# Kernel optimization log

Hardware: AMD Instinct MI355X
Metric: run time of the kernel (lower is better)

## Reference

```python
import jax, jax.numpy as jnp
import numpy as np

EPS = 1e-5
TOP_K = 2

def _conv(x, w, pad):
    # x: [B,Cin,H,W], w: [Cout,Cin,kh,kw]
    return jax.lax.conv_general_dilated(
        x, w, (1, 1), [(pad, pad), (pad, pad)],
        dimension_numbers=('NCHW', 'OIHW', 'NCHW'))

def _bn_eval(x, scale, bias):
    # BatchNorm2d in eval mode with running_mean=0, running_var=1
    inv = scale / jnp.sqrt(1.0 + EPS)
    return x * inv[None, :, None, None] + bias[None, :, None, None]

def setup_inputs() -> dict:
    key = jax.random.key(0)
    ks = jax.random.split(key, 8)
    B, C, O, H, W, E, HID = 16, 256, 256, 56, 56, 8, 512  # HID = int(2.0 * C)
    g = lambda k, shape, f: jax.random.normal(k, shape, jnp.float32) * f
    return {
        'x': jax.random.normal(ks[0], (B, C, H, W), jnp.float32),
        # EfficientSpatialRouter: global-avg-pool -> 1x1 conv to E logits
        'router_w': g(ks[1], (E, C), 0.01),
        'router_b': jnp.zeros((E,), jnp.float32),
        # shared expert: 1x1 conv -> BN -> SiLU
        'shared_w': g(ks[2], (O, C, 1, 1), 0.05),
        'shared_scale': jnp.ones((O,), jnp.float32),
        'shared_bias': jnp.zeros((O,), jnp.float32),
        # SimpleExpert per expert: conv3x3 C->HID, BN, SiLU, conv1x1 HID->O, BN
        'w1': g(ks[3], (E, HID, C, 3, 3), 0.02),
        'bn1_scale': jnp.ones((E, HID), jnp.float32),
        'bn1_bias': jnp.zeros((E, HID), jnp.float32),
        'w2': g(ks[4], (E, O, HID, 1, 1), 0.02),
        'bn2_scale': jnp.ones((E, O), jnp.float32),
        'bn2_bias': jnp.zeros((E, O), jnp.float32),
    }

def reference(x, router_w, router_b, shared_w, shared_scale, shared_bias,
              w1, bn1_scale, bn1_bias, w2, bn2_scale, bn2_bias):
    E = router_w.shape[0]
    # --- routing: pooled features -> logits -> softmax -> top-k renormalized ---
    pooled = x.mean(axis=(2, 3))                          # [B,C]
    logits = pooled @ router_w.T + router_b               # [B,E]
    probs = jax.nn.softmax(logits, axis=-1)
    topk_vals, topk_idx = jax.lax.top_k(probs, TOP_K)     # [B,K]
    weights = topk_vals / topk_vals.sum(axis=-1, keepdims=True)
    # --- shared expert ---
    shared = jax.nn.silu(_bn_eval(_conv(x, shared_w, 0), shared_scale, shared_bias))
    # --- expert dispatch/combine (dense-masked equivalent of gather + index_add) ---
    expert_out = jnp.zeros_like(shared)
    for e in range(E):  # fixed small expert count
        gate = jnp.sum(weights * (topk_idx == e), axis=-1)  # [B], 0 if not routed
        h = jax.nn.silu(_bn_eval(_conv(x, w1[e], 1), bn1_scale[e], bn1_bias[e]))
        y = _bn_eval(_conv(h, w2[e], 0), bn2_scale[e], bn2_bias[e])
        expert_out = expert_out + gate[:, None, None, None] * y
    # residual since in_channels == out_channels
    return shared + expert_out + x
```

## Files before the change

kernel.cpp:

```cpp
#include <hip/hip_runtime.h>
#include <hip/hip_bf16.h>

#define B_ 16
#define C_ 256
#define O_ 256
#define P_ 3136
#define E_ 8
#define HID_ 512
#define EPS_ 1e-5f

typedef __attribute__((ext_vector_type(8))) short bf16x8;
typedef __attribute__((ext_vector_type(4))) float f32x4;
typedef __hip_bfloat16 bf16;

__device__ __forceinline__ void gl2lds16(const bf16* g, bf16* l) {
  __builtin_amdgcn_global_load_lds((const __attribute__((address_space(1))) void*)g,
                                   (__attribute__((address_space(3))) void*)l,
                                   16, 0, 0);
}

__global__ __launch_bounds__(256) void xT_kernel(const float* __restrict__ x,
                                                 bf16* __restrict__ xT,
                                                 float* __restrict__ pooled) {
  __shared__ float tile[64][65];
  const int p0 = blockIdx.x * 64, c0 = blockIdx.y * 64, b = blockIdx.z;
  const int t = threadIdx.x;
#pragma unroll
  for (int j = 0; j < 16; ++j) {
    int idx = t + j * 256;
    int cl = idx >> 6, pl = idx & 63;
    tile[cl][pl] = x[(size_t)(b * C_ + c0 + cl) * P_ + p0 + pl];
  }
  __syncthreads();
#pragma unroll
  for (int j = 0; j < 16; ++j) {
    int idx = t + j * 256;
    int pl = idx >> 6, cl = idx & 63;
    xT[(size_t)(b * P_ + p0 + pl) * C_ + c0 + cl] = __float2bfloat16(tile[cl][pl]);
  }
  if (t < 64) {
    float s = 0.f;
#pragma unroll 8
    for (int pl = 0; pl < 64; ++pl) s += tile[t][pl];
    atomicAdd(&pooled[b * C_ + c0 + t], s * (1.0f / P_));
  }
}

__global__ __launch_bounds__(256) void w1cvt_kernel(const float* __restrict__ w1,
                                                    const float* __restrict__ bn1_scale,
                                                    bf16* __restrict__ w1b) {
  const int eh = blockIdx.x;
  const int e = eh >> 9, hid = eh & 511;
  __shared__ float buf[2304];
  const float* src = w1 + (size_t)eh * 2304;
  const int t = threadIdx.x;
  for (int i = t; i < 2304; i += 256) buf[i] = src[i];
  __syncthreads();
  const float inv = bn1_scale[eh] * (1.0f / sqrtf(1.0f + EPS_));
  for (int i = t; i < 2304; i += 256) {
    int rs = i >> 8, c = i & 255;
    w1b[((size_t)(e * 9 + rs) * HID_ + hid) * C_ + c] = __float2bfloat16(buf[c * 9 + rs] * inv);
  }
}

__global__ __launch_bounds__(256) void w2cvt_kernel(const float* __restrict__ w2,
                                                    const float* __restrict__ bn2_scale,
                                                    bf16* __restrict__ w2b) {
  const int i = blockIdx.x * 256 + threadIdx.x;
  const int eo = i >> 9;
  w2b[i] = __float2bfloat16(w2[i] * (bn2_scale[eo] * (1.0f / sqrtf(1.0f + EPS_))));
}

__global__ __launch_bounds__(256) void wshcvt_kernel(const float* __restrict__ wsh,
                                                     const float* __restrict__ sscale,
                                                     bf16* __restrict__ wshb) {
  const int i = blockIdx.x * 256 + threadIdx.x;
  wshb[i] = __float2bfloat16(wsh[i] * (sscale[i >> 8] * (1.0f / sqrtf(1.0f + EPS_))));
}

__global__ __launch_bounds__(256) void router_kernel(const float* __restrict__ pooled,
                                                     const float* __restrict__ rw,
                                                     const float* __restrict__ rb,
                                                     const float* __restrict__ bn2_bias,
                                                     int* __restrict__ ridx,
                                                     float* __restrict__ rwt,
                                                     float* __restrict__ bsum) {
  __shared__ float lp[B_ * C_];
  __shared__ float llog[B_ * E_];
  __shared__ int lidx[B_ * 2];
  __shared__ float lw[B_ * 2];
  const int t = threadIdx.x;
  for (int i = t; i < B_ * C_; i += 256) lp[i] = pooled[i];
  __syncthreads();
  if (t < B_ * E_) {
    int b = t >> 3, e = t & 7;
    float s = rb[e];
    for (int c = 0; c < C_; ++c) s += lp[b * C_ + c] * rw[e * C_ + c];
    llog[t] = s;
  }
  __syncthreads();
  if (t < B_) {
    float pr[E_];
    float m = -1e30f;
    for (int e = 0; e < E_; ++e) { pr[e] = llog[t * E_ + e]; m = fmaxf(m, pr[e]); }
    float s = 0.f;
    for (int e = 0; e < E_; ++e) { pr[e] = __expf(pr[e] - m); s += pr[e]; }
    const float is = 1.f / s;
    for (int e = 0; e < E_; ++e) pr[e] *= is;
    int i0 = 0; float v0 = pr[0];
    for (int e = 1; e < E_; ++e) if (pr[e] > v0) { v0 = pr[e]; i0 = e; }
    int i1 = -1; float v1 = -1.f;
    for (int e = 0; e < E_; ++e) if (e != i0 && pr[e] > v1) { v1 = pr[e]; i1 = e; }
    const float wsum = 1.f / (v0 + v1);
    ridx[t * 2] = i0; ridx[t * 2 + 1] = i1;
    rwt[t * 2] = v0 * wsum; rwt[t * 2 + 1] = v1 * wsum;
    lidx[t * 2] = i0; lidx[t * 2 + 1] = i1;
    lw[t * 2] = v0 * wsum; lw[t * 2 + 1] = v1 * wsum;
  }
  __syncthreads();
  for (int i = t; i < B_ * O_; i += 256) {
    int b = i >> 8, o = i & 255;
    bsum[i] = lw[b * 2] * bn2_bias[lidx[b * 2] * O_ + o]
            + lw[b * 2 + 1] * bn2_bias[lidx[b * 2 + 1] * O_ + o];
  }
}

__global__ __launch_bounds__(256) void conv1_kernel(
    const bf16* __restrict__ xT, const bf16* __restrict__ w1b,
    const float* __restrict__ bn1_bias, const int* __restrict__ ridx,
    const float* __restrict__ rwt, const bf16* __restrict__ zp,
    bf16* __restrict__ h) {
  __shared__ __align__(16) bf16 ldsA[2][128 * 32];
  __shared__ __align__(16) bf16 ldsB[2][128 * 32];
  const int t = threadIdx.x;
  const int p0 = blockIdx.x * 128;
  const int h0 = blockIdx.y * 128;
  const int bs = blockIdx.z;
  const int b = bs >> 1;
  const int e = ridx[bs];
  const float wk = rwt[bs];

  const int lane = t & 63, wv = t >> 6;
  const int wm = wv >> 1, wn = wv & 1;
  const int r16 = lane & 15, q = lane >> 4;
  const int kslot = (q ^ (r16 & 3)) * 8;

  const int rA = t >> 2;
  const int cSw = ((t & 3) ^ (rA & 3)) * 8;
  const int pA0 = p0 + rA, pA1 = pA0 + 64;
  const int yA0 = pA0 / 56, xA0 = pA0 - yA0 * 56;
  const int yA1 = pA1 / 56, xA1 = pA1 - yA1 * 56;
  const bool vP1 = (pA1 < P_);
  const bf16* xb = xT + (size_t)b * P_ * C_ + cSw;
  const bf16* wb = w1b + ((size_t)(e * 9) * HID_ + h0 + rA) * C_ + cSw;

  f32x4 acc[4][4] = {};

#define STAGE(buf, s) { \
    const int tap_ = (s) >> 3, c0k_ = ((s) & 7) * 32; \
    const int dr_ = tap_ / 3 - 1, dc_ = tap_ % 3 - 1; \
    const int off_ = dr_ * 56 + dc_; \
    const bool v0_ = ((unsigned)(yA0 + dr_) < 56u) & ((unsigned)(xA0 + dc_) < 56u); \
    const bool v1_ = vP1 & ((unsigned)(yA1 + dr_) < 56u) & ((unsigned)(xA1 + dc_) < 56u); \
    const bf16* a0_ = v0_ ? xb + (size_t)(pA0 + off_) * C_ + c0k_ : zp; \
    const bf16* a1_ = v1_ ? xb + (size_t)(pA1 + off_) * C_ + c0k_ : zp; \
    const bf16* b_ = wb + (size_t)(tap_ * HID_) * C_ + c0k_; \
    gl2lds16(a0_, ldsA[buf] + t * 8); \
    gl2lds16(a1_, ldsA[buf] + 2048 + t * 8); \
    gl2lds16(b_, ldsB[buf] + t * 8); \
    gl2lds16(b_ + 64 * C_, ldsB[buf] + 2048 + t * 8); \
  }

  STAGE(0, 0);
  __syncthreads();
  for (int s = 0; s < 72; ++s) {
    const int cur = s & 1;
    if (s < 71) STAGE(cur ^ 1, s + 1);
    const bf16* lA = ldsA[cur];
    const bf16* lB = ldsB[cur];
    bf16x8 af[4], bfr[4];
#pragma unroll
    for (int i = 0; i < 4; ++i) {
      af[i]  = *(const bf16x8*)(lA + (wm * 64 + i * 16 + r16) * 32 + kslot);
      bfr[i] = *(const bf16x8*)(lB + (wn * 64 + i * 16 + r16) * 32 + kslot);
    }
    __builtin_amdgcn_s_setprio(1);
#pragma unroll
    for (int mi = 0; mi < 4; ++mi)
#pragma unroll
      for (int ni = 0; ni < 4; ++ni)
        acc[mi][ni] = __builtin_amdgcn_mfma_f32_16x16x32_bf16(af[mi], bfr[ni], acc[mi][ni], 0, 0, 0);
    __builtin_amdgcn_s_setprio(0);
    if (s < 71) __syncthreads();
  }
#undef STAGE

  const int rowq = q * 4;
  float bias[4];
#pragma unroll
  for (int ni = 0; ni < 4; ++ni)
    bias[ni] = bn1_bias[e * HID_ + h0 + wn * 64 + ni * 16 + r16];
#pragma unroll
  for (int mi = 0; mi < 4; ++mi) {
#pragma unroll
    for (int i = 0; i < 4; ++i) {
      const int p = p0 + wm * 64 + mi * 16 + rowq + i;
      if (p < P_) {
        const size_t base = ((size_t)bs * P_ + p) * HID_;
#pragma unroll
        for (int ni = 0; ni < 4; ++ni) {
          const int hid = h0 + wn * 64 + ni * 16 + r16;
          float v = acc[mi][ni][i] + bias[ni];
          v = v / (1.f + __expf(-v));
          h[base + hid] = __float2bfloat16(wk * v);
        }
      }
    }
  }
}

__global__ __launch_bounds__(256) void combine_kernel(
    const bf16* __restrict__ xT, const bf16* __restrict__ h,
    const bf16* __restrict__ wshb, const bf16* __restrict__ w2b,
    const float* __restrict__ sbias, const float* __restrict__ bsum,
    const int* __restrict__ ridx, const float* __restrict__ x,
    const bf16* __restrict__ zp, float* __restrict__ out) {
  __shared__ __align__(16) bf16 ldsA[2][128 * 32];
  __shared__ __align__(16) bf16 ldsB[2][128 * 32];
  const int t = threadIdx.x;
  const int p0 = blockIdx.x * 128;
  const int o0 = blockIdx.y * 128;
  const int b = blockIdx.z;
  const int e0 = ridx[b * 2], e1 = ridx[b * 2 + 1];

  const int lane = t & 63, wv = t >> 6;
  const int wm = wv >> 1, wn = wv & 1;
  const int r16 = lane & 15, q = lane >> 4;
  const int kslot = (q ^ (r16 & 3)) * 8;

  const int rA = t >> 2;
  const int cSw = ((t & 3) ^ (rA & 3)) * 8;
  const int pB0 = p0 + rA, pB1 = pB0 + 64;
  const bool vB1 = (pB1 < P_);
  const bf16* shA = wshb + (size_t)(o0 + rA) * C_ + cSw;
  const bf16* xB = xT + (size_t)b * P_ * C_ + cSw;

  f32x4 acc[4][4] = {};

#define CSTAGE(buf, s) { \
    if ((s) < 8) { \
      const int c0k_ = (s) * 32; \
      gl2lds16(shA + c0k_, ldsA[buf] + t * 8); \
      gl2lds16(shA + 64 * C_ + c0k_, ldsA[buf] + 2048 + t * 8); \
      gl2lds16(xB + (size_t)pB0 * C_ + c0k_, ldsB[buf] + t * 8); \
      gl2lds16(vB1 ? xB + (size_t)pB1 * C_ + c0k_ : zp, ldsB[buf] + 2048 + t * 8); \
    } else { \
      const int ss_ = (s) - 8; const int slot_ = ss_ >> 4; const int c0k_ = (ss_ & 15) * 32; \
      const int ee_ = slot_ ? e1 : e0; \
      const bf16* wA_ = w2b + ((size_t)(ee_ * O_) + o0 + rA) * HID_ + c0k_ + cSw; \
      const bf16* hB_ = h + ((size_t)(b * 2 + slot_) * P_) * HID_ + c0k_ + cSw; \
      gl2lds16(wA_, ldsA[buf] + t * 8); \
      gl2lds16(wA_ + 64 * HID_, ldsA[buf] + 2048 + t * 8); \
      gl2lds16(hB_ + (size_t)pB0 * HID_, ldsB[buf] + t * 8); \
      gl2lds16(vB1 ? hB_ + (size_t)pB1 * HID_ : zp, ldsB[buf] + 2048 + t * 8); \
    } \
  }

  CSTAGE(0, 0);
  __syncthreads();
  for (int s = 0; s < 40; ++s) {
    const int cur = s & 1;
    if (s < 39) CSTAGE(cur ^ 1, s + 1);
    const bf16* lA = ldsA[cur];
    const bf16* lB = ldsB[cur];
    bf16x8 af[4], bfr[4];
#pragma unroll
    for (int i = 0; i < 4; ++i) {
      af[i]  = *(const bf16x8*)(lA + (wm * 64 + i * 16 + r16) * 32 + kslot);
      bfr[i] = *(const bf16x8*)(lB + (wn * 64 + i * 16 + r16) * 32 + kslot);
    }
    __builtin_amdgcn_s_setprio(1);
#pragma unroll
    for (int mi = 0; mi < 4; ++mi)
#pragma unroll
      for (int ni = 0; ni < 4; ++ni)
        acc[mi][ni] = __builtin_amdgcn_mfma_f32_16x16x32_bf16(af[mi], bfr[ni], acc[mi][ni], 0, 0, 0);
    __builtin_amdgcn_s_setprio(0);
    if (s == 7) {
      const int rowq_ = q * 4;
#pragma unroll
      for (int mi = 0; mi < 4; ++mi)
#pragma unroll
        for (int i = 0; i < 4; ++i) {
          const float bias_ = sbias[o0 + wm * 64 + mi * 16 + rowq_ + i];
#pragma unroll
          for (int ni = 0; ni < 4; ++ni) {
            float v = acc[mi][ni][i] + bias_;
            acc[mi][ni][i] = v / (1.f + __expf(-v));
          }
        }
    }
    if (s < 39) __syncthreads();
  }
#undef CSTAGE

  const int rowq = q * 4;
#pragma unroll
  for (int mi = 0; mi < 4; ++mi) {
#pragma unroll
    for (int i = 0; i < 4; ++i) {
      const int o = o0 + wm * 64 + mi * 16 + rowq + i;
      const float bb = bsum[b * O_ + o];
      const size_t orow = (size_t)(b * O_ + o) * P_;
#pragma unroll
      for (int ni = 0; ni < 4; ++ni) {
        const int p = p0 + wn * 64 + ni * 16 + r16;
        if (p < P_) out[orow + p] = acc[mi][ni][i] + bb + x[orow + p];
      }
    }
  }
}

constexpr size_t SZ_XT = (size_t)B_ * P_ * C_ * 2;
constexpr size_t SZ_W1B = (size_t)E_ * 9 * HID_ * C_ * 2;
constexpr size_t SZ_W2B = (size_t)E_ * O_ * HID_ * 2;
constexpr size_t SZ_WSHB = (size_t)O_ * C_ * 2;
constexpr size_t SZ_POOL = (size_t)B_ * C_ * 4;
constexpr size_t SZ_BSUM = (size_t)B_ * O_ * 4;
constexpr size_t SZ_H = (size_t)B_ * 2 * P_ * HID_ * 2;

constexpr size_t OFF_XT = 0;
constexpr size_t OFF_W1B = OFF_XT + SZ_XT;
constexpr size_t OFF_W2B = OFF_W1B + SZ_W1B;
constexpr size_t OFF_WSHB = OFF_W2B + SZ_W2B;
constexpr size_t OFF_POOL = OFF_WSHB + SZ_WSHB;
constexpr size_t OFF_RIDX = OFF_POOL + SZ_POOL;
constexpr size_t OFF_RWT = OFF_RIDX + 128;
constexpr size_t OFF_BSUM = OFF_RWT + 128;
constexpr size_t OFF_ZERO = OFF_BSUM + SZ_BSUM;
constexpr size_t OFF_H = OFF_ZERO + 1024;

extern "C" void kernel_launch(void* const* d_in, const int* in_sizes, int n_in,
                              void* d_out, int out_size, void* d_ws, size_t ws_size,
                              hipStream_t stream) {
  const float* x = (const float*)d_in[0];
  const float* router_w = (const float*)d_in[1];
  const float* router_b = (const float*)d_in[2];
  const float* shared_w = (const float*)d_in[3];
  const float* shared_scale = (const float*)d_in[4];
  const float* shared_bias = (const float*)d_in[5];
  const float* w1 = (const float*)d_in[6];
  const float* bn1_scale = (const float*)d_in[7];
  const float* bn1_bias = (const float*)d_in[8];
  const float* w2 = (const float*)d_in[9];
  const float* bn2_scale = (const float*)d_in[10];
  const float* bn2_bias = (const float*)d_in[11];
  float* out = (float*)d_out;
  char* ws = (char*)d_ws;

  bf16* xT = (bf16*)(ws + OFF_XT);
  bf16* w1b = (bf16*)(ws + OFF_W1B);
  bf16* w2b = (bf16*)(ws + OFF_W2B);
  bf16* wshb = (bf16*)(ws + OFF_WSHB);
  float* pooled = (float*)(ws + OFF_POOL);
  int* ridx = (int*)(ws + OFF_RIDX);
  float* rwt = (float*)(ws + OFF_RWT);
  float* bsum = (float*)(ws + OFF_BSUM);
  bf16* zp = (bf16*)(ws + OFF_ZERO);
  bf16* h = (bf16*)(ws + OFF_H);

  hipMemsetAsync(ws + OFF_POOL, 0, SZ_POOL, stream);
  hipMemsetAsync(ws + OFF_ZERO, 0, 1024, stream);

  xT_kernel<<<dim3(49, 4, 16), 256, 0, stream>>>(x, xT, pooled);
  w1cvt_kernel<<<E_ * HID_, 256, 0, stream>>>(w1, bn1_scale, w1b);
  w2cvt_kernel<<<(E_ * O_ * HID_) / 256, 256, 0, stream>>>(w2, bn2_scale, w2b);
  wshcvt_kernel<<<(O_ * C_) / 256, 256, 0, stream>>>(shared_w, shared_scale, wshb);
  router_kernel<<<1, 256, 0, stream>>>(pooled, router_w, router_b, bn2_bias, ridx, rwt, bsum);
  conv1_kernel<<<dim3(25, 4, 32), 256, 0, stream>>>(xT, w1b, bn1_bias, ridx, rwt, zp, h);
  combine_kernel<<<dim3(25, 2, 16), 256, 0, stream>>>(xT, h, wshb, w2b, shared_bias, bsum, ridx, x, zp, out);
}
```

Measured before the change: 675.5 us.

## Enlarge GEMM tiles, use K=64 triple-buffered LDS pipeline and XCD-aware block mapping

Both conv1 and combine kernels move to 512-thread blocks with larger output tiles: 256x128 in conv1, and all 256 output channels x 128 pixels in combine. The K-step grows to 64 with a 3-stage LDS ring, and the per-step full barrier is replaced by explicit vmcnt waits plus s_barrier. Blocks are remapped onto a 1D grid so that each XCD handles a contiguous set of batch slots, which should improve L2 reuse of activations and expert weights. The goal is more MFMA work per byte loaded and fewer barriers. In exchange, about 147KB of LDS per block allows only one block per CU, so occupancy is reduced and latency hiding rests on the deeper pipeline.

```diff
diff --git a/kernel.cpp b/kernel.cpp
--- a/kernel.cpp
+++ b/kernel.cpp
@@ -17,6 +17,10 @@
   __builtin_amdgcn_global_load_lds((const __attribute__((address_space(1))) void*)g,
                                    (__attribute__((address_space(3))) void*)l,
                                    16, 0, 0);
+}
+
+__device__ __forceinline__ f32x4 mfma16(bf16x8 a, bf16x8 b, f32x4 c) {
+  return __builtin_amdgcn_mfma_f32_16x16x32_bf16(a, b, c, 0, 0, 0);
 }
 
 __global__ __launch_bounds__(256) void xT_kernel(const float* __restrict__ x,
@@ -125,17 +129,20 @@
   }
 }
 
-__global__ __launch_bounds__(256) void conv1_kernel(
+__global__ __launch_bounds__(512, 2) void conv1_kernel(
     const bf16* __restrict__ xT, const bf16* __restrict__ w1b,
     const float* __restrict__ bn1_bias, const int* __restrict__ ridx,
     const float* __restrict__ rwt, const bf16* __restrict__ zp,
     bf16* __restrict__ h) {
-  __shared__ __align__(16) bf16 ldsA[2][128 * 32];
-  __shared__ __align__(16) bf16 ldsB[2][128 * 32];
+  __shared__ __align__(16) bf16 ldsA[3][256 * 64];
+  __shared__ __align__(16) bf16 ldsB[3][128 * 64];
   const int t = threadIdx.x;
-  const int p0 = blockIdx.x * 128;
-  const int h0 = blockIdx.y * 128;
-  const int bs = blockIdx.z;
+  const int bid = blockIdx.x;
+  const int xcd = bid & 7, j = bid >> 3;
+  const int bsl = j / 52, tile = j % 52;
+  const int mt = tile % 13, nt = tile / 13;
+  const int bs = xcd * 4 + bsl;
+  const int p0 = mt * 256, h0 = nt * 128;
   const int b = bs >> 1;
   const int e = ridx[bs];
   const float wk = rwt[bs];
@@ -143,57 +150,81 @@
   const int lane = t & 63, wv = t >> 6;
   const int wm = wv >> 1, wn = wv & 1;
   const int r16 = lane & 15, q = lane >> 4;
-  const int kslot = (q ^ (r16 & 3)) * 8;
-
-  const int rA = t >> 2;
-  const int cSw = ((t & 3) ^ (rA & 3)) * 8;
-  const int pA0 = p0 + rA, pA1 = pA0 + 64;
-  const int yA0 = pA0 / 56, xA0 = pA0 - yA0 * 56;
-  const int yA1 = pA1 / 56, xA1 = pA1 - yA1 * 56;
-  const bool vP1 = (pA1 < P_);
-  const bf16* xb = xT + (size_t)b * P_ * C_ + cSw;
-  const bf16* wb = w1b + ((size_t)(e * 9) * HID_ + h0 + rA) * C_ + cSw;
+
+  const int srow = t >> 3;
+  const int cho = ((t & 7) ^ (srow & 7)) * 8;
+  int pA[4], yA[4], xA[4];
+#pragma unroll
+  for (int r = 0; r < 4; ++r) {
+    pA[r] = p0 + r * 64 + srow;
+    yA[r] = pA[r] / 56;
+    xA[r] = pA[r] - yA[r] * 56;
+  }
+  const bf16* xb = xT + (size_t)b * P_ * C_ + cho;
+  const bf16* wb = w1b + ((size_t)(e * 9) * HID_ + h0 + srow) * C_ + cho;
+  bf16* laT = &ldsA[0][0] + t * 8;
+  bf16* lbT = &ldsB[0][0] + t * 8;
+
+  auto STAGE = [&](int bf, int s) {
+    const int tap = s >> 2, ck = (s & 3) * 64;
+    const int dr = tap / 3 - 1, dc = tap % 3 - 1;
+    const int off = dr * 56 + dc;
+#pragma unroll
+    for (int r = 0; r < 4; ++r) {
+      const bool v = (pA[r] < P_) & ((unsigned)(yA[r] + dr) < 56u) & ((unsigned)(xA[r] + dc) < 56u);
+      const bf16* sp = v ? xb + (size_t)(pA[r] + off) * C_ + ck : zp;
+      gl2lds16(sp, laT + bf * 16384 + r * 4096);
+    }
+    const bf16* wsrc = wb + (size_t)tap * HID_ * C_ + ck;
+    gl2lds16(wsrc, lbT + bf * 8192);
+    gl2lds16(wsrc + 64 * C_, lbT + bf * 8192 + 4096);
+  };
 
   f32x4 acc[4][4] = {};
 
-#define STAGE(buf, s) { \
-    const int tap_ = (s) >> 3, c0k_ = ((s) & 7) * 32; \
-    const int dr_ = tap_ / 3 - 1, dc_ = tap_ % 3 - 1; \
-    const int off_ = dr_ * 56 + dc_; \
-    const bool v0_ = ((unsigned)(yA0 + dr_) < 56u) & ((unsigned)(xA0 + dc_) < 56u); \
-    const bool v1_ = vP1 & ((unsigned)(yA1 + dr_) < 56u) & ((unsigned)(xA1 + dc_) < 56u); \
-    const bf16* a0_ = v0_ ? xb + (size_t)(pA0 + off_) * C_ + c0k_ : zp; \
-    const bf16* a1_ = v1_ ? xb + (size_t)(pA1 + off_) * C_ + c0k_ : zp; \
-    const bf16* b_ = wb + (size_t)(tap_ * HID_) * C_ + c0k_; \
-    gl2lds16(a0_, ldsA[buf] + t * 8); \
-    gl2lds16(a1_, ldsA[buf] + 2048 + t * 8); \
-    gl2lds16(b_, ldsB[buf] + t * 8); \
-    gl2lds16(b_ + 64 * C_, ldsB[buf] + 2048 + t * 8); \
-  }
-
   STAGE(0, 0);
-  __syncthreads();
-  for (int s = 0; s < 72; ++s) {
-    const int cur = s & 1;
-    if (s < 71) STAGE(cur ^ 1, s + 1);
-    const bf16* lA = ldsA[cur];
-    const bf16* lB = ldsB[cur];
-    bf16x8 af[4], bfr[4];
+  STAGE(1, 1);
+  asm volatile("s_waitcnt vmcnt(6)" ::: "memory");
+  __builtin_amdgcn_s_barrier();
+  asm volatile("" ::: "memory");
+
+  const int Abase = (wm * 64 + r16) * 64;
+  const int Bbase = (wn * 64 + r16) * 64;
+  const int sb0 = (q ^ (r16 & 7)) * 8;
+  const int sb1 = ((4 + q) ^ (r16 & 7)) * 8;
+  int cb = 0;
+  for (int kt = 0; kt < 36; ++kt) {
+    if (kt < 34) {
+      const int nbf = cb + 2 >= 3 ? cb - 1 : cb + 2;
+      STAGE(nbf, kt + 2);
+    }
+    const bf16* lA = &ldsA[0][0] + cb * 16384;
+    const bf16* lB = &ldsB[0][0] + cb * 8192;
+    bf16x8 a0[4], a1[4], b0v[4], b1v[4];
 #pragma unroll
     for (int i = 0; i < 4; ++i) {
-      af[i]  = *(const bf16x8*)(lA + (wm * 64 + i * 16 + r16) * 32 + kslot);
-      bfr[i] = *(const bf16x8*)(lB + (wn * 64 + i * 16 + r16) * 32 + kslot);
+      a0[i] = *(const bf16x8*)(lA + Abase + i * 1024 + sb0);
+      a1[i] = *(const bf16x8*)(lA + Abase + i * 1024 + sb1);
+      b0v[i] = *(const bf16x8*)(lB + Bbase + i * 1024 + sb0);
+      b1v[i] = *(const bf16x8*)(lB + Bbase + i * 1024 + sb1);
     }
     __builtin_amdgcn_s_setprio(1);
 #pragma unroll
     for (int mi = 0; mi < 4; ++mi)
 #pragma unroll
-      for (int ni = 0; ni < 4; ++ni)
-        acc[mi][ni] = __builtin_amdgcn_mfma_f32_16x16x32_bf16(af[mi], bfr[ni], acc[mi][ni], 0, 0, 0);
+      for (int ni = 0; ni < 4; ++ni) {
+        acc[mi][ni] = mfma16(a0[mi], b0v[ni], acc[mi][ni]);
+        acc[mi][ni] = mfma16(a1[mi], b1v[ni], acc[mi][ni]);
+      }
     __builtin_amdgcn_s_setprio(0);
-    if (s < 71) __syncthreads();
-  }
-#undef STAGE
+    if (kt < 35) {
+      if (kt < 34) asm volatile("s_waitcnt vmcnt(6)" ::: "memory");
+      else         asm volatile("s_waitcnt vmcnt(0)" ::: "memory");
+      __builtin_amdgcn_s_barrier();
+      asm volatile("" ::: "memory");
+    }
+    cb = cb + 1 >= 3 ? 0 : cb + 1;
+  }
 
   const int rowq = q * 4;
   float bias[4];
@@ -219,97 +250,137 @@
   }
 }
 
-__global__ __launch_bounds__(256) void combine_kernel(
+__global__ __launch_bounds__(512, 2) void combine_kernel(
     const bf16* __restrict__ xT, const bf16* __restrict__ h,
     const bf16* __restrict__ wshb, const bf16* __restrict__ w2b,
     const float* __restrict__ sbias, const float* __restrict__ bsum,
     const int* __restrict__ ridx, const float* __restrict__ x,
     const bf16* __restrict__ zp, float* __restrict__ out) {
-  __shared__ __align__(16) bf16 ldsA[2][128 * 32];
-  __shared__ __align__(16) bf16 ldsB[2][128 * 32];
+  __shared__ __align__(16) bf16 ldsA[3][256 * 64];
+  __shared__ __align__(16) bf16 ldsB[3][128 * 64];
   const int t = threadIdx.x;
-  const int p0 = blockIdx.x * 128;
-  const int o0 = blockIdx.y * 128;
-  const int b = blockIdx.z;
+  const int bid = blockIdx.x;
+  const int xcd = bid & 7, j = bid >> 3;
+  const int bl = j / 25, pt = j % 25;
+  const int b = xcd * 2 + bl;
+  const int p0 = pt * 128;
   const int e0 = ridx[b * 2], e1 = ridx[b * 2 + 1];
 
   const int lane = t & 63, wv = t >> 6;
   const int wm = wv >> 1, wn = wv & 1;
   const int r16 = lane & 15, q = lane >> 4;
-  const int kslot = (q ^ (r16 & 3)) * 8;
-
-  const int rA = t >> 2;
-  const int cSw = ((t & 3) ^ (rA & 3)) * 8;
-  const int pB0 = p0 + rA, pB1 = pB0 + 64;
-  const bool vB1 = (pB1 < P_);
-  const bf16* shA = wshb + (size_t)(o0 + rA) * C_ + cSw;
-  const bf16* xB = xT + (size_t)b * P_ * C_ + cSw;
+
+  const int srow = t >> 3;
+  const int cho = ((t & 7) ^ (srow & 7)) * 8;
+  int pB[2];
+  pB[0] = p0 + srow;
+  pB[1] = p0 + 64 + srow;
+  const bf16* wshp = wshb + (size_t)srow * C_ + cho;
+  const bf16* w2p0 = w2b + ((size_t)(e0 * O_) + srow) * HID_ + cho;
+  const bf16* w2p1 = w2b + ((size_t)(e1 * O_) + srow) * HID_ + cho;
+  const bf16* xp = xT + (size_t)b * P_ * C_ + cho;
+  const bf16* hp0 = h + (size_t)(b * 2) * P_ * HID_ + cho;
+  const bf16* hp1 = h + (size_t)(b * 2 + 1) * P_ * HID_ + cho;
+  bf16* laT = &ldsA[0][0] + t * 8;
+  bf16* lbT = &ldsB[0][0] + t * 8;
+
+  auto CSTAGE = [&](int bf, int s) {
+    if (s < 4) {
+      const int ck = s * 64;
+#pragma unroll
+      for (int r = 0; r < 4; ++r)
+        gl2lds16(wshp + (size_t)(r * 64) * C_ + ck, laT + bf * 16384 + r * 4096);
+#pragma unroll
+      for (int r = 0; r < 2; ++r) {
+        const bf16* sp = (pB[r] < P_) ? xp + (size_t)pB[r] * C_ + ck : zp;
+        gl2lds16(sp, lbT + bf * 8192 + r * 4096);
+      }
+    } else {
+      const int ss = s - 4;
+      const int sl = ss >> 3, ck = (ss & 7) * 64;
+      const bf16* wa = sl ? w2p1 : w2p0;
+      const bf16* hb = sl ? hp1 : hp0;
+#pragma unroll
+      for (int r = 0; r < 4; ++r)
+        gl2lds16(wa + (size_t)(r * 64) * HID_ + ck, laT + bf * 16384 + r * 4096);
+#pragma unroll
+      for (int r = 0; r < 2; ++r) {
+        const bf16* sp = (pB[r] < P_) ? hb + (size_t)pB[r] * HID_ + ck : zp;
+        gl2lds16(sp, lbT + bf * 8192 + r * 4096);
+      }
+    }
+  };
+
+  const int rowq = q * 4;
+  float sb_[4][4];
+#pragma unroll
+  for (int mi = 0; mi < 4; ++mi)
+#pragma unroll
+    for (int i = 0; i < 4; ++i)
+      sb_[mi][i] = sbias[wm * 64 + mi * 16 + rowq + i];
 
   f32x4 acc[4][4] = {};
 
-#define CSTAGE(buf, s) { \
-    if ((s) < 8) { \
-      const int c0k_ = (s) * 32; \
-      gl2lds16(shA + c0k_, ldsA[buf] + t * 8); \
-      gl2lds16(shA + 64 * C_ + c0k_, ldsA[buf] + 2048 + t * 8); \
-      gl2lds16(xB + (size_t)pB0 * C_ + c0k_, ldsB[buf] + t * 8); \
-      gl2lds16(vB1 ? xB + (size_t)pB1 * C_ + c0k_ : zp, ldsB[buf] + 2048 + t * 8); \
-    } else { \
-      const int ss_ = (s) - 8; const int slot_ = ss_ >> 4; const int c0k_ = (ss_ & 15) * 32; \
-      const int ee_ = slot_ ? e1 : e0; \
-      const bf16* wA_ = w2b + ((size_t)(ee_ * O_) + o0 + rA) * HID_ + c0k_ + cSw; \
-      const bf16* hB_ = h + ((size_t)(b * 2 + slot_) * P_) * HID_ + c0k_ + cSw; \
-      gl2lds16(wA_, ldsA[buf] + t * 8); \
-      gl2lds16(wA_ + 64 * HID_, ldsA[buf] + 2048 + t * 8); \
-      gl2lds16(hB_ + (size_t)pB0 * HID_, ldsB[buf] + t * 8); \
-      gl2lds16(vB1 ? hB_ + (size_t)pB1 * HID_ : zp, ldsB[buf] + 2048 + t * 8); \
-    } \
-  }
-
   CSTAGE(0, 0);
-  __syncthreads();
-  for (int s = 0; s < 40; ++s) {
-    const int cur = s & 1;
-    if (s < 39) CSTAGE(cur ^ 1, s + 1);
-    const bf16* lA = ldsA[cur];
-    const bf16* lB = ldsB[cur];
-    bf16x8 af[4], bfr[4];
+  CSTAGE(1, 1);
+  asm volatile("s_waitcnt vmcnt(6)" ::: "memory");
+  __builtin_amdgcn_s_barrier();
+  asm volatile("" ::: "memory");
+
+  const int Abase = (wm * 64 + r16) * 64;
+  const int Bbase = (wn * 64 + r16) * 64;
+  const int sb0 = (q ^ (r16 & 7)) * 8;
+  const int sb1 = ((4 + q) ^ (r16 & 7)) * 8;
+  int cb = 0;
+  for (int kt = 0; kt < 20; ++kt) {
+    if (kt < 18) {
+      const int nbf = cb + 2 >= 3 ? cb - 1 : cb + 2;
+      CSTAGE(nbf, kt + 2);
+    }
+    const bf16* lA = &ldsA[0][0] + cb * 16384;
+    const bf16* lB = &ldsB[0][0] + cb * 8192;
+    bf16x8 a0[4], a1[4], b0v[4], b1v[4];
 #pragma unroll
     for (int i = 0; i < 4; ++i) {
-      af[i]  = *(const bf16x8*)(lA + (wm * 64 + i * 16 + r16) * 32 + kslot);
-      bfr[i] = *(const bf16x8*)(lB + (wn * 64 + i * 16 + r16) * 32 + kslot);
+      a0[i] = *(const bf16x8*)(lA + Abase + i * 1024 + sb0);
+      a1[i] = *(const bf16x8*)(lA + Abase + i * 1024 + sb1);
+      b0v[i] = *(const bf16x8*)(lB + Bbase + i * 1024 + sb0);
+      b1v[i] = *(const bf16x8*)(lB + Bbase + i * 1024 + sb1);
     }
     __builtin_amdgcn_s_setprio(1);
 #pragma unroll
     for (int mi = 0; mi < 4; ++mi)
 #pragma unroll
-      for (int ni = 0; ni < 4; ++ni)
-        acc[mi][ni] = __builtin_amdgcn_mfma_f32_16x16x32_bf16(af[mi], bfr[ni], acc[mi][ni], 0, 0, 0);
+      for (int ni = 0; ni < 4; ++ni) {
+        acc[mi][ni] = mfma16(a0[mi], b0v[ni], acc[mi][ni]);
+        acc[mi][ni] = mfma16(a1[mi], b1v[ni], acc[mi][ni]);
+      }
     __builtin_amdgcn_s_setprio(0);
-    if (s == 7) {
-      const int rowq_ = q * 4;
+    if (kt == 3) {
 #pragma unroll
       for (int mi = 0; mi < 4; ++mi)
 #pragma unroll
-        for (int i = 0; i < 4; ++i) {
-          const float bias_ = sbias[o0 + wm * 64 + mi * 16 + rowq_ + i];
+        for (int i = 0; i < 4; ++i)
 #pragma unroll
           for (int ni = 0; ni < 4; ++ni) {
-            float v = acc[mi][ni][i] + bias_;
+            float v = acc[mi][ni][i] + sb_[mi][i];
             acc[mi][ni][i] = v / (1.f + __expf(-v));
           }
-        }
-    }
-    if (s < 39) __syncthreads();
-  }
-#undef CSTAGE
-
-  const int rowq = q * 4;
+    }
+    if (kt < 19) {
+      if (kt < 18) asm volatile("s_waitcnt vmcnt(6)" ::: "memory");
+      else         asm volatile("s_waitcnt vmcnt(0)" ::: "memory");
+      __builtin_amdgcn_s_barrier();
+      asm volatile("" ::: "memory");
+    }
+    cb = cb + 1 >= 3 ? 0 : cb + 1;
+  }
+
 #pragma unroll
   for (int mi = 0; mi < 4; ++mi) {
 #pragma unroll
     for (int i = 0; i < 4; ++i) {
-      const int o = o0 + wm * 64 + mi * 16 + rowq + i;
+      const int o = wm * 64 + mi * 16 + rowq + i;
       const float bb = bsum[b * O_ + o];
       const size_t orow = (size_t)(b * O_ + o) * P_;
 #pragma unroll
@@ -327,7 +398,6 @@
 constexpr size_t SZ_WSHB = (size_t)O_ * C_ * 2;
 constexpr size_t SZ_POOL = (size_t)B_ * C_ * 4;
 constexpr size_t SZ_BSUM = (size_t)B_ * O_ * 4;
-constexpr size_t SZ_H = (size_t)B_ * 2 * P_ * HID_ * 2;
 
 constexpr size_t OFF_XT = 0;
 constexpr size_t OFF_W1B = OFF_XT + SZ_XT;
@@ -377,6 +447,6 @@
   w2cvt_kernel<<<(E_ * O_ * HID_) / 256, 256, 0, stream>>>(w2, bn2_scale, w2b);
   wshcvt_kernel<<<(O_ * C_) / 256, 256, 0, stream>>>(shared_w, shared_scale, wshb);
   router_kernel<<<1, 256, 0, stream>>>(pooled, router_w, router_b, bn2_bias, ridx, rwt, bsum);
-  conv1_kernel<<<dim3(25, 4, 32), 256, 0, stream>>>(xT, w1b, bn1_bias, ridx, rwt, zp, h);
-  combine_kernel<<<dim3(25, 2, 16), 256, 0, stream>>>(xT, h, wshb, w2b, shared_bias, bsum, ridx, x, zp, out);
-}
+  conv1_kernel<<<1664, 512, 0, stream>>>(xT, w1b, bn1_bias, ridx, rwt, zp, h);
+  combine_kernel<<<400, 512, 0, stream>>>(xT, h, wshb, w2b, shared_bias, bsum, ridx, x, zp, out);
+}
```

New measurement: 628.9 us. 1.07x faster.

## Use 256x256 tiles, 8-wave blocks, XCD-aware block mapping and finer-grained pipelining

Applied to the files above, without the earlier changes.

Both GEMM kernels (conv1 and combine) move from 128x128 tiles with 4 waves to 256x256 tiles with 8 waves (512 threads) and K-chunks of 64. The main loop is restructured into half-tile interleaved stages with explicit vmcnt waits and raw barriers, so global-to-LDS loads overlap MFMA work. Block indices are remapped so that blocks sharing the same batch/expert land on the same XCD, for L2 reuse. The cost is heavier register pressure (8x4 accumulators) and 128KB of LDS per block, which limits occupancy and adds more barriers per K-step.

```diff
diff --git a/kernel.cpp b/kernel.cpp
--- a/kernel.cpp
+++ b/kernel.cpp
@@ -17,6 +17,10 @@
   __builtin_amdgcn_global_load_lds((const __attribute__((address_space(1))) void*)g,
                                    (__attribute__((address_space(3))) void*)l,
                                    16, 0, 0);
+}
+
+__device__ __forceinline__ f32x4 mfma16(bf16x8 a, bf16x8 b, f32x4 c) {
+  return __builtin_amdgcn_mfma_f32_16x16x32_bf16(a, b, c, 0, 0, 0);
 }
 
 __global__ __launch_bounds__(256) void xT_kernel(const float* __restrict__ x,
@@ -125,75 +129,125 @@
   }
 }
 
-__global__ __launch_bounds__(256) void conv1_kernel(
+
+#define BARX() do { asm volatile("" ::: "memory"); __builtin_amdgcn_s_barrier(); \
+                    asm volatile("" ::: "memory"); } while (0)
+
+#define LOADA(D, H, KS) do { \
+  const bf16* p_ = lds + ((D)*4 + wm) * 8192 + (H) * 4096 + arow + sw##KS; \
+  af[0] = *(const bf16x8*)(p_); \
+  af[1] = *(const bf16x8*)(p_ + 1024); \
+  af[2] = *(const bf16x8*)(p_ + 2048); \
+  af[3] = *(const bf16x8*)(p_ + 3072); \
+} while (0)
+
+#define LOADB(D, KS) do { \
+  const bf16* p_ = lds + ((D)*4 + 2 + bhalf) * 8192 + brow + sw##KS; \
+  bq[0] = *(const bf16x8*)(p_); \
+  bq[1] = *(const bf16x8*)(p_ + 1024); \
+  bq[2] = *(const bf16x8*)(p_ + 2048); \
+  bq[3] = *(const bf16x8*)(p_ + 3072); \
+} while (0)
+
+#define MM(BB) do { \
+  __builtin_amdgcn_s_setprio(1); \
+  acc[(BB)+0][0]=mfma16(af[0],bq[0],acc[(BB)+0][0]); acc[(BB)+0][1]=mfma16(af[0],bq[1],acc[(BB)+0][1]); \
+  acc[(BB)+0][2]=mfma16(af[0],bq[2],acc[(BB)+0][2]); acc[(BB)+0][3]=mfma16(af[0],bq[3],acc[(BB)+0][3]); \
+  acc[(BB)+1][0]=mfma16(af[1],bq[0],acc[(BB)+1][0]); acc[(BB)+1][1]=mfma16(af[1],bq[1],acc[(BB)+1][1]); \
+  acc[(BB)+1][2]=mfma16(af[1],bq[2],acc[(BB)+1][2]); acc[(BB)+1][3]=mfma16(af[1],bq[3],acc[(BB)+1][3]); \
+  acc[(BB)+2][0]=mfma16(af[2],bq[0],acc[(BB)+2][0]); acc[(BB)+2][1]=mfma16(af[2],bq[1],acc[(BB)+2][1]); \
+  acc[(BB)+2][2]=mfma16(af[2],bq[2],acc[(BB)+2][2]); acc[(BB)+2][3]=mfma16(af[2],bq[3],acc[(BB)+2][3]); \
+  acc[(BB)+3][0]=mfma16(af[3],bq[0],acc[(BB)+3][0]); acc[(BB)+3][1]=mfma16(af[3],bq[1],acc[(BB)+3][1]); \
+  acc[(BB)+3][2]=mfma16(af[3],bq[2],acc[(BB)+3][2]); acc[(BB)+3][3]=mfma16(af[3],bq[3],acc[(BB)+3][3]); \
+  __builtin_amdgcn_s_setprio(0); \
+} while (0)
+
+__global__ __launch_bounds__(512, 2) void conv1_kernel(
     const bf16* __restrict__ xT, const bf16* __restrict__ w1b,
     const float* __restrict__ bn1_bias, const int* __restrict__ ridx,
     const float* __restrict__ rwt, const bf16* __restrict__ zp,
     bf16* __restrict__ h) {
-  __shared__ __align__(16) bf16 ldsA[2][128 * 32];
-  __shared__ __align__(16) bf16 ldsB[2][128 * 32];
+  __shared__ __align__(16) bf16 lds[65536];
   const int t = threadIdx.x;
-  const int p0 = blockIdx.x * 128;
-  const int h0 = blockIdx.y * 128;
-  const int bs = blockIdx.z;
+  const int bid = blockIdx.x;
+  const int xcd = bid & 7, j = bid >> 3;
+  const int bs = xcd * 4 + j / 26;
+  const int j2 = j % 26;
+  const int mt = j2 % 13, nt = j2 / 13;
+  const int p0 = mt * 256, h0 = nt * 256;
   const int b = bs >> 1;
   const int e = ridx[bs];
   const float wk = rwt[bs];
 
   const int lane = t & 63, wv = t >> 6;
-  const int wm = wv >> 1, wn = wv & 1;
+  const int wm = wv >> 2, wn = wv & 3;
   const int r16 = lane & 15, q = lane >> 4;
-  const int kslot = (q ^ (r16 & 3)) * 8;
-
-  const int rA = t >> 2;
-  const int cSw = ((t & 3) ^ (rA & 3)) * 8;
-  const int pA0 = p0 + rA, pA1 = pA0 + 64;
-  const int yA0 = pA0 / 56, xA0 = pA0 - yA0 * 56;
-  const int yA1 = pA1 / 56, xA1 = pA1 - yA1 * 56;
-  const bool vP1 = (pA1 < P_);
-  const bf16* xb = xT + (size_t)b * P_ * C_ + cSw;
-  const bf16* wb = w1b + ((size_t)(e * 9) * HID_ + h0 + rA) * C_ + cSw;
-
-  f32x4 acc[4][4] = {};
-
-#define STAGE(buf, s) { \
-    const int tap_ = (s) >> 3, c0k_ = ((s) & 7) * 32; \
-    const int dr_ = tap_ / 3 - 1, dc_ = tap_ % 3 - 1; \
-    const int off_ = dr_ * 56 + dc_; \
-    const bool v0_ = ((unsigned)(yA0 + dr_) < 56u) & ((unsigned)(xA0 + dc_) < 56u); \
-    const bool v1_ = vP1 & ((unsigned)(yA1 + dr_) < 56u) & ((unsigned)(xA1 + dc_) < 56u); \
-    const bf16* a0_ = v0_ ? xb + (size_t)(pA0 + off_) * C_ + c0k_ : zp; \
-    const bf16* a1_ = v1_ ? xb + (size_t)(pA1 + off_) * C_ + c0k_ : zp; \
-    const bf16* b_ = wb + (size_t)(tap_ * HID_) * C_ + c0k_; \
-    gl2lds16(a0_, ldsA[buf] + t * 8); \
-    gl2lds16(a1_, ldsA[buf] + 2048 + t * 8); \
-    gl2lds16(b_, ldsB[buf] + t * 8); \
-    gl2lds16(b_ + 64 * C_, ldsB[buf] + 2048 + t * 8); \
-  }
-
-  STAGE(0, 0);
-  __syncthreads();
-  for (int s = 0; s < 72; ++s) {
-    const int cur = s & 1;
-    if (s < 71) STAGE(cur ^ 1, s + 1);
-    const bf16* lA = ldsA[cur];
-    const bf16* lB = ldsB[cur];
-    bf16x8 af[4], bfr[4];
-#pragma unroll
-    for (int i = 0; i < 4; ++i) {
-      af[i]  = *(const bf16x8*)(lA + (wm * 64 + i * 16 + r16) * 32 + kslot);
-      bfr[i] = *(const bf16x8*)(lB + (wn * 64 + i * 16 + r16) * 32 + kslot);
-    }
-    __builtin_amdgcn_s_setprio(1);
-#pragma unroll
-    for (int mi = 0; mi < 4; ++mi)
-#pragma unroll
-      for (int ni = 0; ni < 4; ++ni)
-        acc[mi][ni] = __builtin_amdgcn_mfma_f32_16x16x32_bf16(af[mi], bfr[ni], acc[mi][ni], 0, 0, 0);
-    __builtin_amdgcn_s_setprio(0);
-    if (s < 71) __syncthreads();
-  }
-#undef STAGE
+  const int bhalf = wn >> 1;
+  const int arow = r16 * 64;
+  const int brow = (wn & 1) * 4096 + arow;
+  const int sw0 = ((q) ^ (r16 & 7)) * 8;
+  const int sw1 = ((4 + q) ^ (r16 & 7)) * 8;
+
+  const int srow = t >> 3;
+  const int cho = ((t & 7) ^ (srow & 7)) * 8;
+  int pA[4], yA[4], xA[4];
+#pragma unroll
+  for (int r = 0; r < 4; ++r) {
+    pA[r] = p0 + r * 64 + srow;
+    yA[r] = pA[r] / 56;
+    xA[r] = pA[r] - yA[r] * 56;
+  }
+  const bf16* xb = xT + (size_t)b * P_ * C_ + cho;
+  const bf16* wb = w1b + ((size_t)(e * 9) * HID_ + h0 + srow) * C_ + cho;
+  bf16* lt = lds + t * 8;
+
+#define STAGEA(HALF, KT) do { \
+  const int tap_ = (KT) >> 2, ck_ = ((KT) & 3) * 64; \
+  const int dr_ = ((tap_ * 11) >> 5) - 1; \
+  const int dc_ = tap_ - (dr_ + 1) * 3 - 1; \
+  const int off_ = dr_ * 56 + dc_; \
+  bf16* d_ = lt + (((KT)&1)*4 + (HALF)) * 8192; \
+  { const bool v_ = (pA[(HALF)*2] < P_) & ((unsigned)(yA[(HALF)*2]+dr_) < 56u) & ((unsigned)(xA[(HALF)*2]+dc_) < 56u); \
+    gl2lds16(v_ ? xb + (size_t)(pA[(HALF)*2]+off_)*C_ + ck_ : zp, d_); } \
+  { const bool v_ = (pA[(HALF)*2+1] < P_) & ((unsigned)(yA[(HALF)*2+1]+dr_) < 56u) & ((unsigned)(xA[(HALF)*2+1]+dc_) < 56u); \
+    gl2lds16(v_ ? xb + (size_t)(pA[(HALF)*2+1]+off_)*C_ + ck_ : zp, d_ + 4096); } \
+} while (0)
+
+#define STAGEB(HALF, KT) do { \
+  const int tap_ = (KT) >> 2, ck_ = ((KT) & 3) * 64; \
+  bf16* d_ = lt + (((KT)&1)*4 + 2 + (HALF)) * 8192; \
+  const bf16* s_ = wb + ((size_t)tap_ * HID_ + (HALF)*128) * C_ + ck_; \
+  gl2lds16(s_, d_); \
+  gl2lds16(s_ + (size_t)64 * C_, d_ + 4096); \
+} while (0)
+
+  f32x4 acc[8][4] = {};
+  bf16x8 af[4], bq[4];
+
+  STAGEA(0, 0); STAGEB(0, 0); STAGEA(1, 0); STAGEB(1, 0); STAGEA(0, 1);
+  asm volatile("s_waitcnt vmcnt(2)" ::: "memory");
+  BARX();
+
+  for (int it = 0; it < 18; ++it) {
+    const int k1 = 2 * it + 1, k2 = 2 * it + 2, k3 = 2 * it + 3;
+    const bool s2 = (k2 < 36), s3 = (k3 < 36);
+    LOADA(0, 0, 0); LOADB(0, 0); STAGEB(0, k1); BARX(); MM(0); BARX();
+    LOADA(0, 1, 0); STAGEA(1, k1); BARX(); MM(4); BARX();
+    LOADA(0, 0, 1); LOADB(0, 1); STAGEB(1, k1); BARX(); MM(0); BARX();
+    LOADA(0, 1, 1); if (s2) STAGEA(0, k2); BARX(); MM(4);
+    if (s2) asm volatile("s_waitcnt vmcnt(2)" ::: "memory");
+    else    asm volatile("s_waitcnt vmcnt(0)" ::: "memory");
+    BARX();
+    LOADA(1, 0, 0); LOADB(1, 0); if (s2) STAGEB(0, k2); BARX(); MM(0); BARX();
+    LOADA(1, 1, 0); if (s2) STAGEA(1, k2); BARX(); MM(4); BARX();
+    LOADA(1, 0, 1); LOADB(1, 1); if (s2) STAGEB(1, k2); BARX(); MM(0); BARX();
+    LOADA(1, 1, 1); if (s3) STAGEA(0, k3); BARX(); MM(4);
+    if (s3) asm volatile("s_waitcnt vmcnt(2)" ::: "memory");
+    else    asm volatile("s_waitcnt vmcnt(0)" ::: "memory");
+    BARX();
+  }
+#undef STAGEA
+#undef STAGEB
 
   const int rowq = q * 4;
   float bias[4];
@@ -201,10 +255,10 @@
   for (int ni = 0; ni < 4; ++ni)
     bias[ni] = bn1_bias[e * HID_ + h0 + wn * 64 + ni * 16 + r16];
 #pragma unroll
-  for (int mi = 0; mi < 4; ++mi) {
+  for (int mi = 0; mi < 8; ++mi) {
 #pragma unroll
     for (int i = 0; i < 4; ++i) {
-      const int p = p0 + wm * 64 + mi * 16 + rowq + i;
+      const int p = p0 + wm * 128 + mi * 16 + rowq + i;
       if (p < P_) {
         const size_t base = ((size_t)bs * P_ + p) * HID_;
 #pragma unroll
@@ -219,80 +273,98 @@
   }
 }
 
-__global__ __launch_bounds__(256) void combine_kernel(
+__global__ __launch_bounds__(512, 2) void combine_kernel(
     const bf16* __restrict__ xT, const bf16* __restrict__ h,
     const bf16* __restrict__ wshb, const bf16* __restrict__ w2b,
     const float* __restrict__ sbias, const float* __restrict__ bsum,
     const int* __restrict__ ridx, const float* __restrict__ x,
     const bf16* __restrict__ zp, float* __restrict__ out) {
-  __shared__ __align__(16) bf16 ldsA[2][128 * 32];
-  __shared__ __align__(16) bf16 ldsB[2][128 * 32];
+  __shared__ __align__(16) bf16 lds[65536];
   const int t = threadIdx.x;
-  const int p0 = blockIdx.x * 128;
-  const int o0 = blockIdx.y * 128;
-  const int b = blockIdx.z;
+  const int bid = blockIdx.x;
+  const int xcd = bid & 7, j = bid >> 3;
+  const int b = xcd * 2 + j / 13;
+  const int pt = j % 13;
+  const int p0 = pt * 256;
   const int e0 = ridx[b * 2], e1 = ridx[b * 2 + 1];
 
   const int lane = t & 63, wv = t >> 6;
-  const int wm = wv >> 1, wn = wv & 1;
+  const int wm = wv >> 2, wn = wv & 3;
   const int r16 = lane & 15, q = lane >> 4;
-  const int kslot = (q ^ (r16 & 3)) * 8;
-
-  const int rA = t >> 2;
-  const int cSw = ((t & 3) ^ (rA & 3)) * 8;
-  const int pB0 = p0 + rA, pB1 = pB0 + 64;
-  const bool vB1 = (pB1 < P_);
-  const bf16* shA = wshb + (size_t)(o0 + rA) * C_ + cSw;
-  const bf16* xB = xT + (size_t)b * P_ * C_ + cSw;
-
-  f32x4 acc[4][4] = {};
-
-#define CSTAGE(buf, s) { \
-    if ((s) < 8) { \
-      const int c0k_ = (s) * 32; \
-      gl2lds16(shA + c0k_, ldsA[buf] + t * 8); \
-      gl2lds16(shA + 64 * C_ + c0k_, ldsA[buf] + 2048 + t * 8); \
-      gl2lds16(xB + (size_t)pB0 * C_ + c0k_, ldsB[buf] + t * 8); \
-      gl2lds16(vB1 ? xB + (size_t)pB1 * C_ + c0k_ : zp, ldsB[buf] + 2048 + t * 8); \
-    } else { \
-      const int ss_ = (s) - 8; const int slot_ = ss_ >> 4; const int c0k_ = (ss_ & 15) * 32; \
-      const int ee_ = slot_ ? e1 : e0; \
-      const bf16* wA_ = w2b + ((size_t)(ee_ * O_) + o0 + rA) * HID_ + c0k_ + cSw; \
-      const bf16* hB_ = h + ((size_t)(b * 2 + slot_) * P_) * HID_ + c0k_ + cSw; \
-      gl2lds16(wA_, ldsA[buf] + t * 8); \
-      gl2lds16(wA_ + 64 * HID_, ldsA[buf] + 2048 + t * 8); \
-      gl2lds16(hB_ + (size_t)pB0 * HID_, ldsB[buf] + t * 8); \
-      gl2lds16(vB1 ? hB_ + (size_t)pB1 * HID_ : zp, ldsB[buf] + 2048 + t * 8); \
-    } \
-  }
-
-  CSTAGE(0, 0);
-  __syncthreads();
-  for (int s = 0; s < 40; ++s) {
-    const int cur = s & 1;
-    if (s < 39) CSTAGE(cur ^ 1, s + 1);
-    const bf16* lA = ldsA[cur];
-    const bf16* lB = ldsB[cur];
-    bf16x8 af[4], bfr[4];
-#pragma unroll
-    for (int i = 0; i < 4; ++i) {
-      af[i]  = *(const bf16x8*)(lA + (wm * 64 + i * 16 + r16) * 32 + kslot);
-      bfr[i] = *(const bf16x8*)(lB + (wn * 64 + i * 16 + r16) * 32 + kslot);
-    }
-    __builtin_amdgcn_s_setprio(1);
-#pragma unroll
-    for (int mi = 0; mi < 4; ++mi)
-#pragma unroll
-      for (int ni = 0; ni < 4; ++ni)
-        acc[mi][ni] = __builtin_amdgcn_mfma_f32_16x16x32_bf16(af[mi], bfr[ni], acc[mi][ni], 0, 0, 0);
-    __builtin_amdgcn_s_setprio(0);
-    if (s == 7) {
-      const int rowq_ = q * 4;
-#pragma unroll
-      for (int mi = 0; mi < 4; ++mi)
+  const int bhalf = wn >> 1;
+  const int arow = r16 * 64;
+  const int brow = (wn & 1) * 4096 + arow;
+  const int sw0 = ((q) ^ (r16 & 7)) * 8;
+  const int sw1 = ((4 + q) ^ (r16 & 7)) * 8;
+
+  const int srow = t >> 3;
+  const int cho = ((t & 7) ^ (srow & 7)) * 8;
+  int pB[4];
+#pragma unroll
+  for (int r = 0; r < 4; ++r) pB[r] = p0 + r * 64 + srow;
+  const bf16* wshp = wshb + (size_t)srow * C_ + cho;
+  const bf16* w2p0 = w2b + ((size_t)(e0 * O_) + srow) * HID_ + cho;
+  const bf16* w2p1 = w2b + ((size_t)(e1 * O_) + srow) * HID_ + cho;
+  const bf16* xp = xT + (size_t)b * P_ * C_ + cho;
+  const bf16* hp0 = h + (size_t)(b * 2) * P_ * HID_ + cho;
+  const bf16* hp1 = h + (size_t)(b * 2 + 1) * P_ * HID_ + cho;
+  bf16* lt = lds + t * 8;
+
+#define CSTAGEA(HALF, KT) do { \
+  bf16* d_ = lt + (((KT)&1)*4 + (HALF)) * 8192; \
+  const bf16* s0_; \
+  size_t rstep_; \
+  if ((KT) < 4)       { s0_ = wshp + (size_t)((HALF)*128)*C_   + (KT)*64;      rstep_ = (size_t)64*C_; } \
+  else if ((KT) < 12) { s0_ = w2p0 + (size_t)((HALF)*128)*HID_ + ((KT)-4)*64;  rstep_ = (size_t)64*HID_; } \
+  else                { s0_ = w2p1 + (size_t)((HALF)*128)*HID_ + ((KT)-12)*64; rstep_ = (size_t)64*HID_; } \
+  gl2lds16(s0_, d_); \
+  gl2lds16(s0_ + rstep_, d_ + 4096); \
+} while (0)
+
+#define CSTAGEB(HALF, KT) do { \
+  bf16* d_ = lt + (((KT)&1)*4 + 2 + (HALF)) * 8192; \
+  if ((KT) < 4) { const int ck_ = (KT)*64; \
+    gl2lds16(pB[(HALF)*2] < P_ ? xp + (size_t)pB[(HALF)*2]*C_ + ck_ : zp, d_); \
+    gl2lds16(pB[(HALF)*2+1] < P_ ? xp + (size_t)pB[(HALF)*2+1]*C_ + ck_ : zp, d_ + 4096); \
+  } else { \
+    const bf16* hb_ = (KT) < 12 ? hp0 : hp1; \
+    const int ck_ = ((KT) < 12 ? (KT)-4 : (KT)-12) * 64; \
+    gl2lds16(pB[(HALF)*2] < P_ ? hb_ + (size_t)pB[(HALF)*2]*HID_ + ck_ : zp, d_); \
+    gl2lds16(pB[(HALF)*2+1] < P_ ? hb_ + (size_t)pB[(HALF)*2+1]*HID_ + ck_ : zp, d_ + 4096); \
+  } \
+} while (0)
+
+  const int rowq = q * 4;
+  f32x4 acc[8][4] = {};
+  bf16x8 af[4], bq[4];
+
+  CSTAGEA(0, 0); CSTAGEB(0, 0); CSTAGEA(1, 0); CSTAGEB(1, 0); CSTAGEA(0, 1);
+  asm volatile("s_waitcnt vmcnt(2)" ::: "memory");
+  BARX();
+
+  for (int it = 0; it < 10; ++it) {
+    const int k1 = 2 * it + 1, k2 = 2 * it + 2, k3 = 2 * it + 3;
+    const bool s2 = (k2 < 20), s3 = (k3 < 20);
+    LOADA(0, 0, 0); LOADB(0, 0); CSTAGEB(0, k1); BARX(); MM(0); BARX();
+    LOADA(0, 1, 0); CSTAGEA(1, k1); BARX(); MM(4); BARX();
+    LOADA(0, 0, 1); LOADB(0, 1); CSTAGEB(1, k1); BARX(); MM(0); BARX();
+    LOADA(0, 1, 1); if (s2) CSTAGEA(0, k2); BARX(); MM(4);
+    if (s2) asm volatile("s_waitcnt vmcnt(2)" ::: "memory");
+    else    asm volatile("s_waitcnt vmcnt(0)" ::: "memory");
+    BARX();
+    LOADA(1, 0, 0); LOADB(1, 0); if (s2) CSTAGEB(0, k2); BARX(); MM(0); BARX();
+    LOADA(1, 1, 0); if (s2) CSTAGEA(1, k2); BARX(); MM(4); BARX();
+    LOADA(1, 0, 1); LOADB(1, 1); if (s2) CSTAGEB(1, k2); BARX(); MM(0); BARX();
+    LOADA(1, 1, 1); if (s3) CSTAGEA(0, k3); BARX(); MM(4);
+    if (s3) asm volatile("s_waitcnt vmcnt(2)" ::: "memory");
+    else    asm volatile("s_waitcnt vmcnt(0)" ::: "memory");
+    BARX();
+    if (it == 1) {
+#pragma unroll
+      for (int mi = 0; mi < 8; ++mi)
 #pragma unroll
         for (int i = 0; i < 4; ++i) {
-          const float bias_ = sbias[o0 + wm * 64 + mi * 16 + rowq_ + i];
+          const float bias_ = sbias[wm * 128 + mi * 16 + rowq + i];
 #pragma unroll
           for (int ni = 0; ni < 4; ++ni) {
             float v = acc[mi][ni][i] + bias_;
@@ -300,16 +372,15 @@
           }
         }
     }
-    if (s < 39) __syncthreads();
-  }
-#undef CSTAGE
-
-  const int rowq = q * 4;
-#pragma unroll
-  for (int mi = 0; mi < 4; ++mi) {
+  }
+#undef CSTAGEA
+#undef CSTAGEB
+
+#pragma unroll
+  for (int mi = 0; mi < 8; ++mi) {
 #pragma unroll
     for (int i = 0; i < 4; ++i) {
-      const int o = o0 + wm * 64 + mi * 16 + rowq + i;
+      const int o = wm * 128 + mi * 16 + rowq + i;
       const float bb = bsum[b * O_ + o];
       const size_t orow = (size_t)(b * O_ + o) * P_;
 #pragma unroll
@@ -327,7 +398,6 @@
 constexpr size_t SZ_WSHB = (size_t)O_ * C_ * 2;
 constexpr size_t SZ_POOL = (size_t)B_ * C_ * 4;
 constexpr size_t SZ_BSUM = (size_t)B_ * O_ * 4;
-constexpr size_t SZ_H = (size_t)B_ * 2 * P_ * HID_ * 2;
 
 constexpr size_t OFF_XT = 0;
 constexpr size_t OFF_W1B = OFF_XT + SZ_XT;
@@ -377,6 +447,6 @@
   w2cvt_kernel<<<(E_ * O_ * HID_) / 256, 256, 0, stream>>>(w2, bn2_scale, w2b);
   wshcvt_kernel<<<(O_ * C_) / 256, 256, 0, stream>>>(shared_w, shared_scale, wshb);
   router_kernel<<<1, 256, 0, stream>>>(pooled, router_w, router_b, bn2_bias, ridx, rwt, bsum);
-  conv1_kernel<<<dim3(25, 4, 32), 256, 0, stream>>>(xT, w1b, bn1_bias, ridx, rwt, zp, h);
-  combine_kernel<<<dim3(25, 2, 16), 256, 0, stream>>>(xT, h, wshb, w2b, shared_bias, bsum, ridx, x, zp, out);
-}
+  conv1_kernel<<<832, 512, 0, stream>>>(xT, w1b, bn1_bias, ridx, rwt, zp, h);
+  combine_kernel<<<208, 512, 0, stream>>>(xT, h, wshb, w2b, shared_bias, bsum, ridx, x, zp, out);
+}
```

Result: faster. 559.6 us (-17.2%).
